# Kernel optimization log

Hardware: AMD Instinct MI355X
Metric: run time of the kernel (lower is better)

The kernel has to match this reference:

```python
import jax, jax.numpy as jnp
import numpy as np

SWIGLU_ALPHA = 1.702
SWIGLU_LIMIT = 7.0
B, S, H, E, K, I = 2, 2048, 2048, 32, 4, 1024


def setup_inputs() -> dict:
    key = jax.random.key(0)
    ks = jax.random.split(key, 8)
    return {
        "hidden_states": jax.random.normal(ks[0], (B, S, H), jnp.float32),
        "gate_w": jax.random.normal(ks[1], (E, H), jnp.float32) * 0.02,
        "gate_b": jnp.zeros((E,), jnp.float32),
        "w_gate": jax.random.normal(ks[2], (E, H, I), jnp.float32) * 0.02,
        "b_gate": jnp.zeros((E, I), jnp.float32),
        "w_up": jax.random.normal(ks[3], (E, H, I), jnp.float32) * 0.02,
        "b_up": jnp.zeros((E, I), jnp.float32),
        "w_down": jax.random.normal(ks[4], (E, I, H), jnp.float32) * 0.02,
        "b_down": jnp.zeros((E, H), jnp.float32),
    }


def reference(hidden_states, gate_w, gate_b, w_gate, b_gate, w_up, b_up, w_down, b_down):
    Bb, Ss, Hh = hidden_states.shape
    x = hidden_states.reshape(-1, Hh)                      # [T, H]
    # --- gate: top-k logits first, then softmax over the selected subset ---
    logits = x @ gate_w.T + gate_b                         # [T, E]
    topk_logits, topk_idx = jax.lax.top_k(logits, K)       # sorted descending
    topk_weight = jax.nn.softmax(topk_logits.astype(jnp.float32), axis=-1)  # [T, K]
    # --- dispatch: replicate each token K times, sort by expert id ---
    flat_idx = topk_idx.reshape(-1)                        # [T*K]
    xs = jnp.repeat(x, K, axis=0)                          # [T*K, H]
    order = jnp.argsort(flat_idx)                          # stable sort by expert
    xt = xs[order]
    gid = flat_idx[order]                                  # expert id per sorted row
    group_sizes = jnp.bincount(flat_idx, length=E).astype(jnp.int32)
    # --- grouped GEMM experts with GPT-OSS SwiGLU ---
    gate = jax.lax.ragged_dot(xt, w_gate, group_sizes) + b_gate[gid]
    up = jax.lax.ragged_dot(xt, w_up, group_sizes) + b_up[gid]
    gate = jnp.minimum(gate, SWIGLU_LIMIT)
    up = jnp.clip(up, -SWIGLU_LIMIT, SWIGLU_LIMIT)
    glu = gate * jax.nn.sigmoid(SWIGLU_ALPHA * gate)
    activated = (up + 1.0) * glu
    outs = jax.lax.ragged_dot(activated, w_down, group_sizes) + b_down[gid]
    # --- unsort and combine with routing weights ---
    inv = jnp.argsort(order)
    outs = outs[inv].reshape(-1, K, Hh)                    # [T, K, H]
    y = jnp.sum(outs * topk_weight[..., None], axis=1).astype(x.dtype)
    return y.reshape(Bb, Ss, Hh)
```

## Files before the change

### kernel.cpp

```cpp
#include <hip/hip_runtime.h>

#define T_TOK 4096
#define E_EXP 32
#define HDIM  2048
#define IDIM  1024
#define TKROW 16384
#define BM    256
#define MAXT  96

typedef __attribute__((ext_vector_type(8))) short   short8;
typedef __attribute__((ext_vector_type(8))) __bf16  bf16x8;
typedef __attribute__((ext_vector_type(4))) float   f32x4;

typedef const __attribute__((address_space(1))) unsigned int* gas_t;
typedef __attribute__((address_space(3))) unsigned int*       las_t;

static __device__ __forceinline__ void gload16(const void* g, void* l) {
    __builtin_amdgcn_global_load_lds((gas_t)(uintptr_t)g, (las_t)(uintptr_t)l, 16, 0, 0);
}

static __device__ __forceinline__ f32x4 mfma16(short8 a, short8 b, f32x4 c) {
    return __builtin_amdgcn_mfma_f32_16x16x32_bf16(
        __builtin_bit_cast(bf16x8, a), __builtin_bit_cast(bf16x8, b), c, 0, 0, 0);
}

static __device__ __forceinline__ unsigned short f2bf(float f) {
    unsigned u = __builtin_bit_cast(unsigned, f);
    unsigned r = (u + 0x7FFFu + ((u >> 16) & 1u)) >> 16;
    return (unsigned short)r;
}
static __device__ __forceinline__ float bf2f(unsigned short u) {
    return __builtin_bit_cast(float, ((unsigned)u) << 16);
}
static __device__ __forceinline__ unsigned cvtpk(float lo, float hi) {
    unsigned r;
    asm("v_cvt_pk_bf16_f32 %0, %1, %2" : "=v"(r) : "v"(lo), "v"(hi));
    return r;
}

#define VM0()   asm volatile("s_waitcnt vmcnt(0)" ::: "memory")
#define LGKM0() asm volatile("s_waitcnt lgkmcnt(0)" ::: "memory")

__global__ __launch_bounds__(256) void gating_kernel(
    const float* __restrict__ x, const float* __restrict__ gw,
    const float* __restrict__ gb, int* __restrict__ topk_idx,
    float* __restrict__ topk_w)
{
    int wave = threadIdx.x >> 6, lane = threadIdx.x & 63;
    int t = blockIdx.x * 4 + wave;
    const float* xr = x + (size_t)t * HDIM;
    float xv[32];
#pragma unroll
    for (int j = 0; j < 32; j++) xv[j] = xr[lane + 64 * j];
    float logits[E_EXP];
#pragma unroll
    for (int e = 0; e < E_EXP; e++) {
        const float* wr = gw + (size_t)e * HDIM;
        float s = 0.f;
#pragma unroll
        for (int j = 0; j < 32; j++) s = fmaf(xv[j], wr[lane + 64 * j], s);
#pragma unroll
        for (int off = 32; off; off >>= 1) s += __shfl_xor(s, off);
        logits[e] = s + gb[e];
    }
    unsigned sel = 0;
    float v[4]; int id[4];
#pragma unroll
    for (int kk = 0; kk < 4; kk++) {
        float best = -3.4e38f; int bi = 0;
#pragma unroll
        for (int e = 0; e < E_EXP; e++) {
            bool ok = ((sel >> e) & 1u) == 0u;
            bool gt = ok && (logits[e] > best);
            best = gt ? logits[e] : best;
            bi   = gt ? e : bi;
        }
        sel |= 1u << bi; v[kk] = best; id[kk] = bi;
    }
    float m0 = v[0];
    float e0 = __expf(v[0] - m0), e1 = __expf(v[1] - m0);
    float e2 = __expf(v[2] - m0), e3 = __expf(v[3] - m0);
    float inv = 1.f / (e0 + e1 + e2 + e3);
    if (lane == 0) {
        int b4 = t * 4;
        topk_idx[b4 + 0] = id[0]; topk_w[b4 + 0] = e0 * inv;
        topk_idx[b4 + 1] = id[1]; topk_w[b4 + 1] = e1 * inv;
        topk_idx[b4 + 2] = id[2]; topk_w[b4 + 2] = e2 * inv;
        topk_idx[b4 + 3] = id[3]; topk_w[b4 + 3] = e3 * inv;
    }
}

__global__ void init_kernel(int* counts, int* fill) {
    if (threadIdx.x < E_EXP) { counts[threadIdx.x] = 0; fill[threadIdx.x] = 0; }
}

__global__ void histo_kernel(const int* __restrict__ idx, int* counts) {
    int i = blockIdx.x * 256 + threadIdx.x;
    atomicAdd(&counts[idx[i]], 1);
}

__global__ void scan_tiles_kernel(const int* counts, int* offsets,
                                  int* tile_e, int* tile_r, int* ntiles) {
    if (threadIdx.x == 0) {
        int acc = 0;
        for (int e = 0; e < E_EXP; e++) { offsets[e] = acc; acc += counts[e]; }
        offsets[E_EXP] = acc;
        int nt = 0;
        for (int e = 0; e < E_EXP; e++) {
            int c = counts[e];
            for (int r = 0; r < c; r += BM) {
                tile_e[nt] = e; tile_r[nt] = offsets[e] + r; nt++;
            }
        }
        ntiles[0] = nt;
    }
}

__global__ void scatter_kernel(const int* __restrict__ idx, const int* __restrict__ offsets,
                               int* fill, int* __restrict__ pos_of, int* __restrict__ row_tok) {
    int i = blockIdx.x * 256 + threadIdx.x;
    int e = idx[i];
    int pos = offsets[e] + atomicAdd(&fill[e], 1);
    pos_of[i] = pos;
    row_tok[pos] = i >> 2;
}

__global__ __launch_bounds__(64) void gather_kernel(
    const float* __restrict__ x, const int* __restrict__ row_tok,
    unsigned short* __restrict__ xt)
{
    int r = blockIdx.x, lane = threadIdx.x;
    const f32x4* src = (const f32x4*)(x + (size_t)row_tok[r] * HDIM);
    unsigned short* dst = xt + (size_t)r * HDIM;
#pragma unroll
    for (int j = 0; j < 8; j++) {
        f32x4 f = src[lane + 64 * j];
        uint2 o;
        o.x = cvtpk(f[0], f[1]);
        o.y = cvtpk(f[2], f[3]);
        *(uint2*)(dst + 4 * (lane + 64 * j)) = o;
    }
}

__global__ __launch_bounds__(512, 2) void gemm1_kernel(
    const unsigned short* __restrict__ xt, const float* __restrict__ w_gate,
    const float* __restrict__ b_gate, const float* __restrict__ w_up,
    const float* __restrict__ b_up, const int* __restrict__ tile_e,
    const int* __restrict__ tile_r, const int* __restrict__ ntiles,
    const int* __restrict__ offsets, const int* __restrict__ counts,
    unsigned short* __restrict__ act)
{
    int flat = blockIdx.y * 8 + blockIdx.x;
    int swz = (flat & 7) * (MAXT * 8 / 8) + (flat >> 3);
    int tid = swz >> 3, nb = swz & 7;
    if (tid >= ntiles[0]) return;
    int e = tile_e[tid], row0 = tile_r[tid];
    int cnt_end = offsets[e] + counts[e];
    int n0 = nb * 128;

    __shared__ unsigned short As[2][BM * 64];
    __shared__ unsigned short Bgs[2][128 * 64];
    __shared__ unsigned short Bus[2][128 * 64];

    int t = threadIdx.x, lane = t & 63, w = t >> 6;
    int wr = w >> 2, wc = w & 3;
    int lrow = lane & 15, lg8 = (lane >> 4) * 8;

    f32x4 accg[8][2], accu[8][2];
#pragma unroll
    for (int m = 0; m < 8; m++)
#pragma unroll
        for (int n = 0; n < 2; n++) { accg[m][n] = (f32x4)0.f; accu[m][n] = (f32x4)0.f; }

    int arow_l = (lane >> 3);
    int achunk = (lane & 7) ^ arow_l;
    int bn = (t & 31) * 4, bk = (t >> 5) * 4;
    int bfswz = ((t & 31) & 7) << 3;
    size_t wB = (size_t)e * ((size_t)HDIM * IDIM) + (size_t)bk * IDIM + n0 + bn;

    f32x4 gReg[4], uReg[4];

#define G1_STAGE_A(KT, BUF) do { int k0_ = (KT) * 64; \
    _Pragma("unroll") for (int i_ = 0; i_ < 4; i_++) { \
        int ar_ = row0 + 32 * w + 8 * i_ + arow_l; \
        if (ar_ > TKROW - 1) ar_ = TKROW - 1; \
        gload16(xt + (size_t)ar_ * HDIM + k0_ + achunk * 8, \
                (void*)&As[BUF][(32 * w + 8 * i_) * 64]); \
    } } while (0)

#define G1_LOADB(KT) do { \
    const float* gp_ = w_gate + wB + (size_t)(KT) * 64 * IDIM; \
    const float* up_ = w_up   + wB + (size_t)(KT) * 64 * IDIM; \
    _Pragma("unroll") for (int kk_ = 0; kk_ < 4; kk_++) { \
        gReg[kk_] = *(const f32x4*)(gp_ + (size_t)kk_ * IDIM); \
        uReg[kk_] = *(const f32x4*)(up_ + (size_t)kk_ * IDIM); \
    } } while (0)

#define G1_WRITEB(BUF) do { \
    _Pragma("unroll") for (int j_ = 0; j_ < 4; j_++) { \
        uint2 vg_, vu_; \
        vg_.x = cvtpk(gReg[0][j_], gReg[1][j_]); vg_.y = cvtpk(gReg[2][j_], gReg[3][j_]); \
        vu_.x = cvtpk(uReg[0][j_], uReg[1][j_]); vu_.y = cvtpk(uReg[2][j_], uReg[3][j_]); \
        int d_ = (bn + j_) * 64 + (bk ^ bfswz); \
        *(uint2*)&Bgs[BUF][d_] = vg_; *(uint2*)&Bus[BUF][d_] = vu_; \
    } } while (0)

#define G1_MFMA(BUF) do { \
    __builtin_amdgcn_s_setprio(1); \
    _Pragma("unroll") for (int kk_ = 0; kk_ < 2; kk_++) { \
        short8 af_[8], bg_[2], bu_[2]; \
        int ke_ = kk_ * 32 + lg8; \
        _Pragma("unroll") for (int m_ = 0; m_ < 8; m_++) \
            af_[m_] = *(const short8*)&As[BUF][(wr * 128 + m_ * 16 + lrow) * 64 + (ke_ ^ ((lrow & 7) << 3))]; \
        _Pragma("unroll") for (int n_ = 0; n_ < 2; n_++) { \
            int rb_ = wc * 32 + n_ * 16 + lrow; \
            int d_ = rb_ * 64 + (ke_ ^ (((rb_ >> 2) & 7) << 3)); \
            bg_[n_] = *(const short8*)&Bgs[BUF][d_]; \
            bu_[n_] = *(const short8*)&Bus[BUF][d_]; \
        } \
        _Pragma("unroll") for (int m_ = 0; m_ < 8; m_++) \
        _Pragma("unroll") for (int n_ = 0; n_ < 2; n_++) { \
            accg[m_][n_] = mfma16(af_[m_], bg_[n_], accg[m_][n_]); \
            accu[m_][n_] = mfma16(af_[m_], bu_[n_], accu[m_][n_]); \
        } \
    } \
    __builtin_amdgcn_s_setprio(0); } while (0)

    G1_STAGE_A(0, 0);
    G1_LOADB(0);
    VM0();
    G1_WRITEB(0);
    LGKM0();
    __builtin_amdgcn_s_barrier();

    int cur = 0;
#pragma unroll 1
    for (int kt = 0; kt < 32; kt++) {
        if (kt + 1 < 32) { G1_STAGE_A(kt + 1, cur ^ 1); G1_LOADB(kt + 1); }
        G1_MFMA(cur);
        VM0();
        if (kt + 1 < 32) G1_WRITEB(cur ^ 1);
        LGKM0();
        __builtin_amdgcn_s_barrier();
        cur ^= 1;
    }
#undef G1_STAGE_A
#undef G1_LOADB
#undef G1_WRITEB
#undef G1_MFMA

#pragma unroll
    for (int nf = 0; nf < 2; nf++) {
        int col = n0 + wc * 32 + nf * 16 + lrow;
        float bgv = b_gate[e * IDIM + col];
        float buv = b_up[e * IDIM + col];
#pragma unroll
        for (int m = 0; m < 8; m++) {
            int rb = row0 + wr * 128 + m * 16 + (lane >> 4) * 4;
#pragma unroll
            for (int r = 0; r < 4; r++) {
                int grow = rb + r;
                if (grow < cnt_end) {
                    float gv = accg[m][nf][r] + bgv;
                    float uv = accu[m][nf][r] + buv;
                    gv = fminf(gv, 7.f);
                    uv = fminf(fmaxf(uv, -7.f), 7.f);
                    float glu = gv / (1.f + __expf(-1.702f * gv));
                    act[(size_t)grow * IDIM + col] = f2bf((uv + 1.f) * glu);
                }
            }
        }
    }
}

__global__ __launch_bounds__(512, 2) void gemm2_kernel(
    const unsigned short* __restrict__ actb, const float* __restrict__ w_down,
    const float* __restrict__ b_down, const int* __restrict__ tile_e,
    const int* __restrict__ tile_r, const int* __restrict__ ntiles,
    const int* __restrict__ offsets, const int* __restrict__ counts,
    unsigned short* __restrict__ outs)
{
    int flat = blockIdx.y * 8 + blockIdx.x;
    int swz = (flat & 7) * (MAXT * 8 / 8) + (flat >> 3);
    int tid = swz >> 3, nb = swz & 7;
    if (tid >= ntiles[0]) return;
    int e = tile_e[tid], row0 = tile_r[tid];
    int cnt_end = offsets[e] + counts[e];
    int n0 = nb * 256;

    __shared__ unsigned short As[2][BM * 64];
    __shared__ unsigned short Bs[2][256 * 64];

    int t = threadIdx.x, lane = t & 63, w = t >> 6;
    int wr = w >> 2, wc = w & 3;
    int lrow = lane & 15, lg8 = (lane >> 4) * 8;

    f32x4 acc[8][4];
#pragma unroll
    for (int m = 0; m < 8; m++)
#pragma unroll
        for (int n = 0; n < 4; n++) acc[m][n] = (f32x4)0.f;

    int arow_l = (lane >> 3);
    int achunk = (lane & 7) ^ arow_l;
    int bn = (t & 63) * 4, bk = w * 8;
    int bfswz = (lane & 7) << 3;
    size_t wB = (size_t)e * ((size_t)IDIM * HDIM) + (size_t)bk * HDIM + n0 + bn;

    f32x4 dReg[8];

#define G2_STAGE_A(KT, BUF) do { int k0_ = (KT) * 64; \
    _Pragma("unroll") for (int i_ = 0; i_ < 4; i_++) { \
        int ar_ = row0 + 32 * w + 8 * i_ + arow_l; \
        if (ar_ > TKROW - 1) ar_ = TKROW - 1; \
        gload16(actb + (size_t)ar_ * IDIM + k0_ + achunk * 8, \
                (void*)&As[BUF][(32 * w + 8 * i_) * 64]); \
    } } while (0)

#define G2_LOADB(KT) do { \
    const float* gp_ = w_down + wB + (size_t)(KT) * 64 * HDIM; \
    _Pragma("unroll") for (int kk_ = 0; kk_ < 8; kk_++) \
        dReg[kk_] = *(const f32x4*)(gp_ + (size_t)kk_ * HDIM); \
    } while (0)

#define G2_WRITEB(BUF) do { \
    _Pragma("unroll") for (int j_ = 0; j_ < 4; j_++) { \
        uint4 v_; \
        v_.x = cvtpk(dReg[0][j_], dReg[1][j_]); v_.y = cvtpk(dReg[2][j_], dReg[3][j_]); \
        v_.z = cvtpk(dReg[4][j_], dReg[5][j_]); v_.w = cvtpk(dReg[6][j_], dReg[7][j_]); \
        int d_ = (bn + j_) * 64 + (bk ^ bfswz); \
        *(uint4*)&Bs[BUF][d_] = v_; \
    } } while (0)

#define G2_MFMA(BUF) do { \
    __builtin_amdgcn_s_setprio(1); \
    _Pragma("unroll") for (int kk_ = 0; kk_ < 2; kk_++) { \
        short8 af_[8], bf_[4]; \
        int ke_ = kk_ * 32 + lg8; \
        _Pragma("unroll") for (int m_ = 0; m_ < 8; m_++) \
            af_[m_] = *(const short8*)&As[BUF][(wr * 128 + m_ * 16 + lrow) * 64 + (ke_ ^ ((lrow & 7) << 3))]; \
        _Pragma("unroll") for (int n_ = 0; n_ < 4; n_++) { \
            int rb_ = wc * 64 + n_ * 16 + lrow; \
            bf_[n_] = *(const short8*)&Bs[BUF][rb_ * 64 + (ke_ ^ (((rb_ >> 2) & 7) << 3))]; \
        } \
        _Pragma("unroll") for (int m_ = 0; m_ < 8; m_++) \
        _Pragma("unroll") for (int n_ = 0; n_ < 4; n_++) \
            acc[m_][n_] = mfma16(af_[m_], bf_[n_], acc[m_][n_]); \
    } \
    __builtin_amdgcn_s_setprio(0); } while (0)

    G2_STAGE_A(0, 0);
    G2_LOADB(0);
    VM0();
    G2_WRITEB(0);
    LGKM0();
    __builtin_amdgcn_s_barrier();

    int cur = 0;
#pragma unroll 1
    for (int kt = 0; kt < 16; kt++) {
        if (kt + 1 < 16) { G2_STAGE_A(kt + 1, cur ^ 1); G2_LOADB(kt + 1); }
        G2_MFMA(cur);
        VM0();
        if (kt + 1 < 16) G2_WRITEB(cur ^ 1);
        LGKM0();
        __builtin_amdgcn_s_barrier();
        cur ^= 1;
    }
#undef G2_STAGE_A
#undef G2_LOADB
#undef G2_WRITEB
#undef G2_MFMA

#pragma unroll
    for (int nf = 0; nf < 4; nf++) {
        int col = n0 + wc * 64 + nf * 16 + lrow;
        float bdv = b_down[e * HDIM + col];
#pragma unroll
        for (int m = 0; m < 8; m++) {
            int rb = row0 + wr * 128 + m * 16 + (lane >> 4) * 4;
#pragma unroll
            for (int r = 0; r < 4; r++) {
                int grow = rb + r;
                if (grow < cnt_end)
                    outs[(size_t)grow * HDIM + col] = f2bf(acc[m][nf][r] + bdv);
            }
        }
    }
}

__global__ __launch_bounds__(256) void combine_kernel(
    const unsigned short* __restrict__ outs, const int* __restrict__ pos_of,
    const float* __restrict__ topk_w, float* __restrict__ y)
{
    int tok = blockIdx.x;
    int c0 = threadIdx.x * 8;
    float acc[8] = {0.f, 0.f, 0.f, 0.f, 0.f, 0.f, 0.f, 0.f};
#pragma unroll
    for (int k = 0; k < 4; k++) {
        int pos = pos_of[tok * 4 + k];
        float w = topk_w[tok * 4 + k];
        short8 vv = *(const short8*)(outs + (size_t)pos * HDIM + c0);
#pragma unroll
        for (int j = 0; j < 8; j++)
            acc[j] = fmaf(w, bf2f((unsigned short)vv[j]), acc[j]);
    }
    float4 o0 = make_float4(acc[0], acc[1], acc[2], acc[3]);
    float4 o1 = make_float4(acc[4], acc[5], acc[6], acc[7]);
    *(float4*)(y + (size_t)tok * HDIM + c0)     = o0;
    *(float4*)(y + (size_t)tok * HDIM + c0 + 4) = o1;
}

extern "C" void kernel_launch(void* const* d_in, const int* in_sizes, int n_in,
                              void* d_out, int out_size, void* d_ws, size_t ws_size,
                              hipStream_t stream) {
    const float* x      = (const float*)d_in[0];
    const float* gw     = (const float*)d_in[1];
    const float* gb     = (const float*)d_in[2];
    const float* w_gate = (const float*)d_in[3];
    const float* b_gate = (const float*)d_in[4];
    const float* w_up   = (const float*)d_in[5];
    const float* b_up   = (const float*)d_in[6];
    const float* w_down = (const float*)d_in[7];
    const float* b_down = (const float*)d_in[8];
    float* y = (float*)d_out;

    char* base = (char*)d_ws;
    size_t off = 0;
    int*   topk_idx = (int*)(base + off);   off += (size_t)TKROW * 4;
    float* topk_w   = (float*)(base + off); off += (size_t)TKROW * 4;
    int*   counts   = (int*)(base + off);   off += 256;
    int*   offsets  = (int*)(base + off);   off += 256;
    int*   fill     = (int*)(base + off);   off += 256;
    int*   ntiles   = (int*)(base + off);   off += 256;
    int*   tile_e   = (int*)(base + off);   off += 1024;
    int*   tile_r   = (int*)(base + off);   off += 1024;
    int*   pos_of   = (int*)(base + off);   off += (size_t)TKROW * 4;
    int*   row_tok  = (int*)(base + off);   off += (size_t)TKROW * 4;
    unsigned short* xt   = (unsigned short*)(base + off); off += (size_t)TKROW * HDIM * 2;
    unsigned short* act  = (unsigned short*)(base + off); off += (size_t)TKROW * IDIM * 2;
    unsigned short* outs = (unsigned short*)(base + off); off += (size_t)TKROW * HDIM * 2;

    init_kernel<<<1, 64, 0, stream>>>(counts, fill);
    gating_kernel<<<T_TOK / 4, 256, 0, stream>>>(x, gw, gb, topk_idx, topk_w);
    histo_kernel<<<TKROW / 256, 256, 0, stream>>>(topk_idx, counts);
    scan_tiles_kernel<<<1, 64, 0, stream>>>(counts, offsets, tile_e, tile_r, ntiles);
    scatter_kernel<<<TKROW / 256, 256, 0, stream>>>(topk_idx, offsets, fill, pos_of, row_tok);
    gather_kernel<<<TKROW, 64, 0, stream>>>(x, row_tok, xt);
    gemm1_kernel<<<dim3(8, MAXT), 512, 0, stream>>>(
        xt, w_gate, b_gate, w_up, b_up, tile_e, tile_r, ntiles, offsets, counts, act);
    gemm2_kernel<<<dim3(8, MAXT), 512, 0, stream>>>(
        act, w_down, b_down, tile_e, tile_r, ntiles, offsets, counts, outs);
    combine_kernel<<<T_TOK, 256, 0, stream>>>(outs, pos_of, topk_w, y);
}
```

Baseline: 622.6 us.

## Halve expert GEMM N-tiles and double-buffer weight register prefetch with partial vmcnt waits

Both grouped-GEMM kernels now use half-width N tiles: 64 columns for gate/up and 128 for down. The grid is doubled and waves are rearranged into a 4x2 layout with smaller accumulator arrays. The weight fp32->bf16 staging now keeps two register sets in flight, prefetching two k-steps ahead. The full vmcnt(0) drains are replaced by counted waits, and a sched_barrier is added after each barrier, so global loads overlap MFMA work. The cost is that the A tile is re-read from memory by twice as many blocks, and the hand-counted waitcnt logic is fragile.

```diff
diff --git a/kernel.cpp b/kernel.cpp
--- a/kernel.cpp
+++ b/kernel.cpp
@@ -37,9 +37,16 @@
     asm("v_cvt_pk_bf16_f32 %0, %1, %2" : "=v"(r) : "v"(lo), "v"(hi));
     return r;
 }
-
-#define VM0()   asm volatile("s_waitcnt vmcnt(0)" ::: "memory")
-#define LGKM0() asm volatile("s_waitcnt lgkmcnt(0)" ::: "memory")
+static __device__ __forceinline__ unsigned cvtpkp(float lo, float hi) {
+    unsigned r;
+    asm volatile("v_cvt_pk_bf16_f32 %0, %1, %2" : "=v"(r) : "v"(lo), "v"(hi) : "memory");
+    return r;
+}
+
+#define FENCE()    asm volatile("" ::: "memory")
+#define WAITVM(N)  asm volatile("s_waitcnt vmcnt(" #N ")" ::: "memory")
+#define LGKM0()    asm volatile("s_waitcnt lgkmcnt(0)" ::: "memory")
+#define BAR()      do { __builtin_amdgcn_s_barrier(); __builtin_amdgcn_sched_barrier(0); } while (0)
 
 __global__ __launch_bounds__(256) void gating_kernel(
     const float* __restrict__ x, const float* __restrict__ gw,
@@ -150,35 +157,34 @@
     const int* __restrict__ offsets, const int* __restrict__ counts,
     unsigned short* __restrict__ act)
 {
-    int flat = blockIdx.y * 8 + blockIdx.x;
-    int swz = (flat & 7) * (MAXT * 8 / 8) + (flat >> 3);
-    int tid = swz >> 3, nb = swz & 7;
+    int flat = blockIdx.y * 16 + blockIdx.x;
+    int swz = (flat & 7) * 192 + (flat >> 3);
+    int tid = swz >> 4, nb = swz & 15;
     if (tid >= ntiles[0]) return;
     int e = tile_e[tid], row0 = tile_r[tid];
     int cnt_end = offsets[e] + counts[e];
-    int n0 = nb * 128;
+    int n0 = nb * 64;
 
     __shared__ unsigned short As[2][BM * 64];
-    __shared__ unsigned short Bgs[2][128 * 64];
-    __shared__ unsigned short Bus[2][128 * 64];
+    __shared__ unsigned short Bg[2][64 * 64];
+    __shared__ unsigned short Bu[2][64 * 64];
 
     int t = threadIdx.x, lane = t & 63, w = t >> 6;
-    int wr = w >> 2, wc = w & 3;
+    int wr = w >> 1, wc = w & 1;
     int lrow = lane & 15, lg8 = (lane >> 4) * 8;
 
-    f32x4 accg[8][2], accu[8][2];
-#pragma unroll
-    for (int m = 0; m < 8; m++)
+    f32x4 accg[4][2], accu[4][2];
+#pragma unroll
+    for (int m = 0; m < 4; m++)
 #pragma unroll
         for (int n = 0; n < 2; n++) { accg[m][n] = (f32x4)0.f; accu[m][n] = (f32x4)0.f; }
 
-    int arow_l = (lane >> 3);
+    int arow_l = lane >> 3;
     int achunk = (lane & 7) ^ arow_l;
-    int bn = (t & 31) * 4, bk = (t >> 5) * 4;
-    int bfswz = ((t & 31) & 7) << 3;
-    size_t wB = (size_t)e * ((size_t)HDIM * IDIM) + (size_t)bk * IDIM + n0 + bn;
-
-    f32x4 gReg[4], uReg[4];
+    int bn4 = (t & 15) * 4, kr2 = (t >> 4) * 2;
+    size_t wB = (size_t)e * ((size_t)HDIM * IDIM) + (size_t)kr2 * IDIM + n0 + bn4;
+
+    f32x4 gS0[2], uS0[2], gS1[2], uS1[2];
 
 #define G1_STAGE_A(KT, BUF) do { int k0_ = (KT) * 64; \
     _Pragma("unroll") for (int i_ = 0; i_ < 4; i_++) { \
@@ -188,62 +194,76 @@
                 (void*)&As[BUF][(32 * w + 8 * i_) * 64]); \
     } } while (0)
 
-#define G1_LOADB(KT) do { \
-    const float* gp_ = w_gate + wB + (size_t)(KT) * 64 * IDIM; \
-    const float* up_ = w_up   + wB + (size_t)(KT) * 64 * IDIM; \
-    _Pragma("unroll") for (int kk_ = 0; kk_ < 4; kk_++) { \
-        gReg[kk_] = *(const f32x4*)(gp_ + (size_t)kk_ * IDIM); \
-        uReg[kk_] = *(const f32x4*)(up_ + (size_t)kk_ * IDIM); \
-    } } while (0)
-
-#define G1_WRITEB(BUF) do { \
+#define G1_LOADB(KT, GV, UV) do { \
+    const float* gp_ = w_gate + wB + (size_t)(KT) * (64 * IDIM); \
+    const float* up_ = w_up   + wB + (size_t)(KT) * (64 * IDIM); \
+    GV[0] = *(const f32x4*)(gp_); GV[1] = *(const f32x4*)(gp_ + IDIM); \
+    UV[0] = *(const f32x4*)(up_); UV[1] = *(const f32x4*)(up_ + IDIM); \
+    } while (0)
+
+#define G1_WRITEB(GV, UV, BUF) do { \
     _Pragma("unroll") for (int j_ = 0; j_ < 4; j_++) { \
-        uint2 vg_, vu_; \
-        vg_.x = cvtpk(gReg[0][j_], gReg[1][j_]); vg_.y = cvtpk(gReg[2][j_], gReg[3][j_]); \
-        vu_.x = cvtpk(uReg[0][j_], uReg[1][j_]); vu_.y = cvtpk(uReg[2][j_], uReg[3][j_]); \
-        int d_ = (bn + j_) * 64 + (bk ^ bfswz); \
-        *(uint2*)&Bgs[BUF][d_] = vg_; *(uint2*)&Bus[BUF][d_] = vu_; \
+        unsigned vg_ = cvtpkp(GV[0][j_], GV[1][j_]); \
+        unsigned vu_ = cvtpkp(UV[0][j_], UV[1][j_]); \
+        int r_ = bn4 + j_; int d_ = r_ * 64 + (kr2 ^ ((r_ & 7) << 3)); \
+        *(unsigned*)&Bg[BUF][d_] = vg_; *(unsigned*)&Bu[BUF][d_] = vu_; \
     } } while (0)
 
 #define G1_MFMA(BUF) do { \
     __builtin_amdgcn_s_setprio(1); \
     _Pragma("unroll") for (int kk_ = 0; kk_ < 2; kk_++) { \
-        short8 af_[8], bg_[2], bu_[2]; \
+        short8 af_[4], bg_[2], bu_[2]; \
         int ke_ = kk_ * 32 + lg8; \
-        _Pragma("unroll") for (int m_ = 0; m_ < 8; m_++) \
-            af_[m_] = *(const short8*)&As[BUF][(wr * 128 + m_ * 16 + lrow) * 64 + (ke_ ^ ((lrow & 7) << 3))]; \
+        _Pragma("unroll") for (int m_ = 0; m_ < 4; m_++) { \
+            int rr_ = wr * 64 + m_ * 16 + lrow; \
+            af_[m_] = *(const short8*)&As[BUF][rr_ * 64 + (ke_ ^ ((rr_ & 7) << 3))]; } \
         _Pragma("unroll") for (int n_ = 0; n_ < 2; n_++) { \
-            int rb_ = wc * 32 + n_ * 16 + lrow; \
-            int d_ = rb_ * 64 + (ke_ ^ (((rb_ >> 2) & 7) << 3)); \
-            bg_[n_] = *(const short8*)&Bgs[BUF][d_]; \
-            bu_[n_] = *(const short8*)&Bus[BUF][d_]; \
-        } \
-        _Pragma("unroll") for (int m_ = 0; m_ < 8; m_++) \
+            int rr_ = wc * 32 + n_ * 16 + lrow; \
+            int d_ = rr_ * 64 + (ke_ ^ ((rr_ & 7) << 3)); \
+            bg_[n_] = *(const short8*)&Bg[BUF][d_]; \
+            bu_[n_] = *(const short8*)&Bu[BUF][d_]; } \
+        _Pragma("unroll") for (int m_ = 0; m_ < 4; m_++) \
         _Pragma("unroll") for (int n_ = 0; n_ < 2; n_++) { \
             accg[m_][n_] = mfma16(af_[m_], bg_[n_], accg[m_][n_]); \
-            accu[m_][n_] = mfma16(af_[m_], bu_[n_], accu[m_][n_]); \
-        } \
+            accu[m_][n_] = mfma16(af_[m_], bu_[n_], accu[m_][n_]); } \
     } \
     __builtin_amdgcn_s_setprio(0); } while (0)
 
-    G1_STAGE_A(0, 0);
-    G1_LOADB(0);
-    VM0();
-    G1_WRITEB(0);
-    LGKM0();
-    __builtin_amdgcn_s_barrier();
+    G1_STAGE_A(0, 0); FENCE();
+    G1_LOADB(0, gS0, uS0); FENCE();
+    G1_LOADB(1, gS1, uS1); FENCE();
+    WAITVM(4);
+    G1_WRITEB(gS0, uS0, 0);
+    LGKM0(); BAR();
 
     int cur = 0;
 #pragma unroll 1
-    for (int kt = 0; kt < 32; kt++) {
-        if (kt + 1 < 32) { G1_STAGE_A(kt + 1, cur ^ 1); G1_LOADB(kt + 1); }
+    for (int kt = 0; kt < 30; kt += 2) {
+        FENCE(); G1_STAGE_A(kt + 1, cur ^ 1); FENCE();
+        G1_LOADB(kt + 2, gS0, uS0); FENCE();
         G1_MFMA(cur);
-        VM0();
-        if (kt + 1 < 32) G1_WRITEB(cur ^ 1);
-        LGKM0();
-        __builtin_amdgcn_s_barrier();
+        WAITVM(8);
+        G1_WRITEB(gS1, uS1, cur ^ 1);
+        WAITVM(4);
+        LGKM0(); BAR();
         cur ^= 1;
-    }
+        FENCE(); G1_STAGE_A(kt + 2, cur ^ 1); FENCE();
+        G1_LOADB(kt + 3, gS1, uS1); FENCE();
+        G1_MFMA(cur);
+        WAITVM(8);
+        G1_WRITEB(gS0, uS0, cur ^ 1);
+        WAITVM(4);
+        LGKM0(); BAR();
+        cur ^= 1;
+    }
+    FENCE(); G1_STAGE_A(31, cur ^ 1); FENCE();
+    G1_MFMA(cur);
+    WAITVM(4);
+    G1_WRITEB(gS1, uS1, cur ^ 1);
+    WAITVM(0);
+    LGKM0(); BAR();
+    cur ^= 1;
+    G1_MFMA(cur);
 #undef G1_STAGE_A
 #undef G1_LOADB
 #undef G1_WRITEB
@@ -255,8 +275,8 @@
         float bgv = b_gate[e * IDIM + col];
         float buv = b_up[e * IDIM + col];
 #pragma unroll
-        for (int m = 0; m < 8; m++) {
-            int rb = row0 + wr * 128 + m * 16 + (lane >> 4) * 4;
+        for (int m = 0; m < 4; m++) {
+            int rb = row0 + wr * 64 + m * 16 + (lane >> 4) * 4;
 #pragma unroll
             for (int r = 0; r < 4; r++) {
                 int grow = rb + r;
@@ -280,34 +300,33 @@
     const int* __restrict__ offsets, const int* __restrict__ counts,
     unsigned short* __restrict__ outs)
 {
-    int flat = blockIdx.y * 8 + blockIdx.x;
-    int swz = (flat & 7) * (MAXT * 8 / 8) + (flat >> 3);
-    int tid = swz >> 3, nb = swz & 7;
+    int flat = blockIdx.y * 16 + blockIdx.x;
+    int swz = (flat & 7) * 192 + (flat >> 3);
+    int tid = swz >> 4, nb = swz & 15;
     if (tid >= ntiles[0]) return;
     int e = tile_e[tid], row0 = tile_r[tid];
     int cnt_end = offsets[e] + counts[e];
-    int n0 = nb * 256;
+    int n0 = nb * 128;
 
     __shared__ unsigned short As[2][BM * 64];
-    __shared__ unsigned short Bs[2][256 * 64];
+    __shared__ unsigned short Bs[2][128 * 64];
 
     int t = threadIdx.x, lane = t & 63, w = t >> 6;
-    int wr = w >> 2, wc = w & 3;
+    int wr = w >> 1, wc = w & 1;
     int lrow = lane & 15, lg8 = (lane >> 4) * 8;
 
-    f32x4 acc[8][4];
-#pragma unroll
-    for (int m = 0; m < 8; m++)
+    f32x4 acc[4][4];
+#pragma unroll
+    for (int m = 0; m < 4; m++)
 #pragma unroll
         for (int n = 0; n < 4; n++) acc[m][n] = (f32x4)0.f;
 
-    int arow_l = (lane >> 3);
+    int arow_l = lane >> 3;
     int achunk = (lane & 7) ^ arow_l;
-    int bn = (t & 63) * 4, bk = w * 8;
-    int bfswz = (lane & 7) << 3;
-    size_t wB = (size_t)e * ((size_t)IDIM * HDIM) + (size_t)bk * HDIM + n0 + bn;
-
-    f32x4 dReg[8];
+    int bn4 = (t & 31) * 4, kr4 = (t >> 5) * 4;
+    size_t wB = (size_t)e * ((size_t)IDIM * HDIM) + (size_t)kr4 * HDIM + n0 + bn4;
+
+    f32x4 dS0[4], dS1[4];
 
 #define G2_STAGE_A(KT, BUF) do { int k0_ = (KT) * 64; \
     _Pragma("unroll") for (int i_ = 0; i_ < 4; i_++) { \
@@ -317,56 +336,72 @@
                 (void*)&As[BUF][(32 * w + 8 * i_) * 64]); \
     } } while (0)
 
-#define G2_LOADB(KT) do { \
-    const float* gp_ = w_down + wB + (size_t)(KT) * 64 * HDIM; \
-    _Pragma("unroll") for (int kk_ = 0; kk_ < 8; kk_++) \
-        dReg[kk_] = *(const f32x4*)(gp_ + (size_t)kk_ * HDIM); \
+#define G2_LOADB(KT, DV) do { \
+    const float* gp_ = w_down + wB + (size_t)(KT) * (64 * HDIM); \
+    DV[0] = *(const f32x4*)(gp_);            DV[1] = *(const f32x4*)(gp_ + HDIM); \
+    DV[2] = *(const f32x4*)(gp_ + 2 * HDIM); DV[3] = *(const f32x4*)(gp_ + 3 * HDIM); \
     } while (0)
 
-#define G2_WRITEB(BUF) do { \
+#define G2_WRITEB(DV, BUF) do { \
     _Pragma("unroll") for (int j_ = 0; j_ < 4; j_++) { \
-        uint4 v_; \
-        v_.x = cvtpk(dReg[0][j_], dReg[1][j_]); v_.y = cvtpk(dReg[2][j_], dReg[3][j_]); \
-        v_.z = cvtpk(dReg[4][j_], dReg[5][j_]); v_.w = cvtpk(dReg[6][j_], dReg[7][j_]); \
-        int d_ = (bn + j_) * 64 + (bk ^ bfswz); \
-        *(uint4*)&Bs[BUF][d_] = v_; \
+        uint2 v_; \
+        v_.x = cvtpkp(DV[0][j_], DV[1][j_]); v_.y = cvtpkp(DV[2][j_], DV[3][j_]); \
+        int r_ = bn4 + j_; int d_ = r_ * 64 + (kr4 ^ ((r_ & 7) << 3)); \
+        *(uint2*)&Bs[BUF][d_] = v_; \
     } } while (0)
 
 #define G2_MFMA(BUF) do { \
     __builtin_amdgcn_s_setprio(1); \
     _Pragma("unroll") for (int kk_ = 0; kk_ < 2; kk_++) { \
-        short8 af_[8], bf_[4]; \
+        short8 af_[4], bf_[4]; \
         int ke_ = kk_ * 32 + lg8; \
-        _Pragma("unroll") for (int m_ = 0; m_ < 8; m_++) \
-            af_[m_] = *(const short8*)&As[BUF][(wr * 128 + m_ * 16 + lrow) * 64 + (ke_ ^ ((lrow & 7) << 3))]; \
+        _Pragma("unroll") for (int m_ = 0; m_ < 4; m_++) { \
+            int rr_ = wr * 64 + m_ * 16 + lrow; \
+            af_[m_] = *(const short8*)&As[BUF][rr_ * 64 + (ke_ ^ ((rr_ & 7) << 3))]; } \
         _Pragma("unroll") for (int n_ = 0; n_ < 4; n_++) { \
-            int rb_ = wc * 64 + n_ * 16 + lrow; \
-            bf_[n_] = *(const short8*)&Bs[BUF][rb_ * 64 + (ke_ ^ (((rb_ >> 2) & 7) << 3))]; \
-        } \
-        _Pragma("unroll") for (int m_ = 0; m_ < 8; m_++) \
+            int rr_ = wc * 64 + n_ * 16 + lrow; \
+            bf_[n_] = *(const short8*)&Bs[BUF][rr_ * 64 + (ke_ ^ ((rr_ & 7) << 3))]; } \
+        _Pragma("unroll") for (int m_ = 0; m_ < 4; m_++) \
         _Pragma("unroll") for (int n_ = 0; n_ < 4; n_++) \
             acc[m_][n_] = mfma16(af_[m_], bf_[n_], acc[m_][n_]); \
     } \
     __builtin_amdgcn_s_setprio(0); } while (0)
 
-    G2_STAGE_A(0, 0);
-    G2_LOADB(0);
-    VM0();
-    G2_WRITEB(0);
-    LGKM0();
-    __builtin_amdgcn_s_barrier();
+    G2_STAGE_A(0, 0); FENCE();
+    G2_LOADB(0, dS0); FENCE();
+    G2_LOADB(1, dS1); FENCE();
+    WAITVM(4);
+    G2_WRITEB(dS0, 0);
+    LGKM0(); BAR();
 
     int cur = 0;
 #pragma unroll 1
-    for (int kt = 0; kt < 16; kt++) {
-        if (kt + 1 < 16) { G2_STAGE_A(kt + 1, cur ^ 1); G2_LOADB(kt + 1); }
+    for (int kt = 0; kt < 14; kt += 2) {
+        FENCE(); G2_STAGE_A(kt + 1, cur ^ 1); FENCE();
+        G2_LOADB(kt + 2, dS0); FENCE();
         G2_MFMA(cur);
-        VM0();
-        if (kt + 1 < 16) G2_WRITEB(cur ^ 1);
-        LGKM0();
-        __builtin_amdgcn_s_barrier();
+        WAITVM(8);
+        G2_WRITEB(dS1, cur ^ 1);
+        WAITVM(4);
+        LGKM0(); BAR();
         cur ^= 1;
-    }
+        FENCE(); G2_STAGE_A(kt + 2, cur ^ 1); FENCE();
+        G2_LOADB(kt + 3, dS1); FENCE();
+        G2_MFMA(cur);
+        WAITVM(8);
+        G2_WRITEB(dS0, cur ^ 1);
+        WAITVM(4);
+        LGKM0(); BAR();
+        cur ^= 1;
+    }
+    FENCE(); G2_STAGE_A(15, cur ^ 1); FENCE();
+    G2_MFMA(cur);
+    WAITVM(4);
+    G2_WRITEB(dS1, cur ^ 1);
+    WAITVM(0);
+    LGKM0(); BAR();
+    cur ^= 1;
+    G2_MFMA(cur);
 #undef G2_STAGE_A
 #undef G2_LOADB
 #undef G2_WRITEB
@@ -377,8 +412,8 @@
         int col = n0 + wc * 64 + nf * 16 + lrow;
         float bdv = b_down[e * HDIM + col];
 #pragma unroll
-        for (int m = 0; m < 8; m++) {
-            int rb = row0 + wr * 128 + m * 16 + (lane >> 4) * 4;
+        for (int m = 0; m < 4; m++) {
+            int rb = row0 + wr * 64 + m * 16 + (lane >> 4) * 4;
 #pragma unroll
             for (int r = 0; r < 4; r++) {
                 int grow = rb + r;
@@ -447,9 +482,9 @@
     scan_tiles_kernel<<<1, 64, 0, stream>>>(counts, offsets, tile_e, tile_r, ntiles);
     scatter_kernel<<<TKROW / 256, 256, 0, stream>>>(topk_idx, offsets, fill, pos_of, row_tok);
     gather_kernel<<<TKROW, 64, 0, stream>>>(x, row_tok, xt);
-    gemm1_kernel<<<dim3(8, MAXT), 512, 0, stream>>>(
+    gemm1_kernel<<<dim3(16, MAXT), 512, 0, stream>>>(
         xt, w_gate, b_gate, w_up, b_up, tile_e, tile_r, ntiles, offsets, counts, act);
-    gemm2_kernel<<<dim3(8, MAXT), 512, 0, stream>>>(
+    gemm2_kernel<<<dim3(16, MAXT), 512, 0, stream>>>(
         act, w_down, b_down, tile_e, tile_r, ntiles, offsets, counts, outs);
     combine_kernel<<<T_TOK, 256, 0, stream>>>(outs, pos_of, topk_w, y);
 }
```

After: 716.8 us. 15.1% more time.

## Deepen B-weight register prefetch to two stages and split MFMA halves around LDS writes

Applied to the files above, without the earlier changes.

Both grouped GEMM kernels now keep two register sets of fp32 weights in flight, loading tile kt+2 while tile kt is computed. Each k-tile's MFMA work is split into two halves, with the bf16 conversion and LDS write of the next B tile placed between them. Partial vmcnt waits replace full drains, and compiler fences plus sched_barrier pin the ordering. This aims to hide global weight-load latency behind MFMA work, at the cost of more VGPRs (possible spills or lower occupancy under launch_bounds(512,2)) and fragile hand-counted waitcnt values.

```diff
diff --git a/kernel.cpp b/kernel.cpp
--- a/kernel.cpp
+++ b/kernel.cpp
@@ -37,9 +37,16 @@
     asm("v_cvt_pk_bf16_f32 %0, %1, %2" : "=v"(r) : "v"(lo), "v"(hi));
     return r;
 }
-
-#define VM0()   asm volatile("s_waitcnt vmcnt(0)" ::: "memory")
-#define LGKM0() asm volatile("s_waitcnt lgkmcnt(0)" ::: "memory")
+static __device__ __forceinline__ unsigned cvtpkp(float lo, float hi) {
+    unsigned r;
+    asm volatile("v_cvt_pk_bf16_f32 %0, %1, %2" : "=v"(r) : "v"(lo), "v"(hi) : "memory");
+    return r;
+}
+
+#define FENCE()    asm volatile("" ::: "memory")
+#define WAITVM(N)  asm volatile("s_waitcnt vmcnt(" #N ")" ::: "memory")
+#define LGKM0()    asm volatile("s_waitcnt lgkmcnt(0)" ::: "memory")
+#define BAR()      do { __builtin_amdgcn_s_barrier(); __builtin_amdgcn_sched_barrier(0); } while (0)
 
 __global__ __launch_bounds__(256) void gating_kernel(
     const float* __restrict__ x, const float* __restrict__ gw,
@@ -151,7 +158,7 @@
     unsigned short* __restrict__ act)
 {
     int flat = blockIdx.y * 8 + blockIdx.x;
-    int swz = (flat & 7) * (MAXT * 8 / 8) + (flat >> 3);
+    int swz = (flat & 7) * (MAXT) + (flat >> 3);
     int tid = swz >> 3, nb = swz & 7;
     if (tid >= ntiles[0]) return;
     int e = tile_e[tid], row0 = tile_r[tid];
@@ -178,7 +185,7 @@
     int bfswz = ((t & 31) & 7) << 3;
     size_t wB = (size_t)e * ((size_t)HDIM * IDIM) + (size_t)bk * IDIM + n0 + bn;
 
-    f32x4 gReg[4], uReg[4];
+    f32x4 gS0[4], uS0[4], gS1[4], uS1[4];
 
 #define G1_STAGE_A(KT, BUF) do { int k0_ = (KT) * 64; \
     _Pragma("unroll") for (int i_ = 0; i_ < 4; i_++) { \
@@ -188,28 +195,28 @@
                 (void*)&As[BUF][(32 * w + 8 * i_) * 64]); \
     } } while (0)
 
-#define G1_LOADB(KT) do { \
+#define G1_LOADB(KT, GV, UV) do { \
     const float* gp_ = w_gate + wB + (size_t)(KT) * 64 * IDIM; \
     const float* up_ = w_up   + wB + (size_t)(KT) * 64 * IDIM; \
     _Pragma("unroll") for (int kk_ = 0; kk_ < 4; kk_++) { \
-        gReg[kk_] = *(const f32x4*)(gp_ + (size_t)kk_ * IDIM); \
-        uReg[kk_] = *(const f32x4*)(up_ + (size_t)kk_ * IDIM); \
+        GV[kk_] = *(const f32x4*)(gp_ + (size_t)kk_ * IDIM); \
+        UV[kk_] = *(const f32x4*)(up_ + (size_t)kk_ * IDIM); \
     } } while (0)
 
-#define G1_WRITEB(BUF) do { \
+#define G1_WRITEB(GV, UV, BUF) do { \
     _Pragma("unroll") for (int j_ = 0; j_ < 4; j_++) { \
         uint2 vg_, vu_; \
-        vg_.x = cvtpk(gReg[0][j_], gReg[1][j_]); vg_.y = cvtpk(gReg[2][j_], gReg[3][j_]); \
-        vu_.x = cvtpk(uReg[0][j_], uReg[1][j_]); vu_.y = cvtpk(uReg[2][j_], uReg[3][j_]); \
+        vg_.x = cvtpkp(GV[0][j_], GV[1][j_]); vg_.y = cvtpkp(GV[2][j_], GV[3][j_]); \
+        vu_.x = cvtpkp(UV[0][j_], UV[1][j_]); vu_.y = cvtpkp(UV[2][j_], UV[3][j_]); \
         int d_ = (bn + j_) * 64 + (bk ^ bfswz); \
         *(uint2*)&Bgs[BUF][d_] = vg_; *(uint2*)&Bus[BUF][d_] = vu_; \
     } } while (0)
 
-#define G1_MFMA(BUF) do { \
+#define G1_MFMA_H(BUF, KK) do { \
     __builtin_amdgcn_s_setprio(1); \
-    _Pragma("unroll") for (int kk_ = 0; kk_ < 2; kk_++) { \
+    { \
         short8 af_[8], bg_[2], bu_[2]; \
-        int ke_ = kk_ * 32 + lg8; \
+        int ke_ = (KK) * 32 + lg8; \
         _Pragma("unroll") for (int m_ = 0; m_ < 8; m_++) \
             af_[m_] = *(const short8*)&As[BUF][(wr * 128 + m_ * 16 + lrow) * 64 + (ke_ ^ ((lrow & 7) << 3))]; \
         _Pragma("unroll") for (int n_ = 0; n_ < 2; n_++) { \
@@ -226,28 +233,46 @@
     } \
     __builtin_amdgcn_s_setprio(0); } while (0)
 
-    G1_STAGE_A(0, 0);
-    G1_LOADB(0);
-    VM0();
-    G1_WRITEB(0);
-    LGKM0();
-    __builtin_amdgcn_s_barrier();
+    G1_STAGE_A(0, 0); FENCE();
+    G1_LOADB(0, gS0, uS0); FENCE();
+    G1_LOADB(1, gS1, uS1); FENCE();
+    WAITVM(8);
+    G1_WRITEB(gS0, uS0, 0);
+    LGKM0(); BAR();
 
     int cur = 0;
 #pragma unroll 1
-    for (int kt = 0; kt < 32; kt++) {
-        if (kt + 1 < 32) { G1_STAGE_A(kt + 1, cur ^ 1); G1_LOADB(kt + 1); }
-        G1_MFMA(cur);
-        VM0();
-        if (kt + 1 < 32) G1_WRITEB(cur ^ 1);
-        LGKM0();
-        __builtin_amdgcn_s_barrier();
-        cur ^= 1;
-    }
+    for (int kt = 0; kt < 30; kt += 2) {
+        FENCE(); G1_STAGE_A(kt + 1, cur ^ 1); FENCE();
+        G1_LOADB(kt + 2, gS0, uS0); FENCE();
+        G1_MFMA_H(cur, 0);
+        WAITVM(12);
+        G1_WRITEB(gS1, uS1, cur ^ 1);
+        G1_MFMA_H(cur, 1);
+        WAITVM(8);
+        LGKM0(); BAR(); cur ^= 1;
+        FENCE(); G1_STAGE_A(kt + 2, cur ^ 1); FENCE();
+        G1_LOADB(kt + 3, gS1, uS1); FENCE();
+        G1_MFMA_H(cur, 0);
+        WAITVM(12);
+        G1_WRITEB(gS0, uS0, cur ^ 1);
+        G1_MFMA_H(cur, 1);
+        WAITVM(8);
+        LGKM0(); BAR(); cur ^= 1;
+    }
+    FENCE(); G1_STAGE_A(31, cur ^ 1); FENCE();
+    G1_MFMA_H(cur, 0);
+    WAITVM(4);
+    G1_WRITEB(gS1, uS1, cur ^ 1);
+    G1_MFMA_H(cur, 1);
+    WAITVM(0);
+    LGKM0(); BAR(); cur ^= 1;
+    G1_MFMA_H(cur, 0);
+    G1_MFMA_H(cur, 1);
 #undef G1_STAGE_A
 #undef G1_LOADB
 #undef G1_WRITEB
-#undef G1_MFMA
+#undef G1_MFMA_H
 
 #pragma unroll
     for (int nf = 0; nf < 2; nf++) {
@@ -281,7 +306,7 @@
     unsigned short* __restrict__ outs)
 {
     int flat = blockIdx.y * 8 + blockIdx.x;
-    int swz = (flat & 7) * (MAXT * 8 / 8) + (flat >> 3);
+    int swz = (flat & 7) * (MAXT) + (flat >> 3);
     int tid = swz >> 3, nb = swz & 7;
     if (tid >= ntiles[0]) return;
     int e = tile_e[tid], row0 = tile_r[tid];
@@ -307,7 +332,7 @@
     int bfswz = (lane & 7) << 3;
     size_t wB = (size_t)e * ((size_t)IDIM * HDIM) + (size_t)bk * HDIM + n0 + bn;
 
-    f32x4 dReg[8];
+    f32x4 dS0[8], dS1[8];
 
 #define G2_STAGE_A(KT, BUF) do { int k0_ = (KT) * 64; \
     _Pragma("unroll") for (int i_ = 0; i_ < 4; i_++) { \
@@ -317,26 +342,26 @@
                 (void*)&As[BUF][(32 * w + 8 * i_) * 64]); \
     } } while (0)
 
-#define G2_LOADB(KT) do { \
+#define G2_LOADB(KT, DV) do { \
     const float* gp_ = w_down + wB + (size_t)(KT) * 64 * HDIM; \
     _Pragma("unroll") for (int kk_ = 0; kk_ < 8; kk_++) \
-        dReg[kk_] = *(const f32x4*)(gp_ + (size_t)kk_ * HDIM); \
+        DV[kk_] = *(const f32x4*)(gp_ + (size_t)kk_ * HDIM); \
     } while (0)
 
-#define G2_WRITEB(BUF) do { \
+#define G2_WRITEB(DV, BUF) do { \
     _Pragma("unroll") for (int j_ = 0; j_ < 4; j_++) { \
         uint4 v_; \
-        v_.x = cvtpk(dReg[0][j_], dReg[1][j_]); v_.y = cvtpk(dReg[2][j_], dReg[3][j_]); \
-        v_.z = cvtpk(dReg[4][j_], dReg[5][j_]); v_.w = cvtpk(dReg[6][j_], dReg[7][j_]); \
+        v_.x = cvtpkp(DV[0][j_], DV[1][j_]); v_.y = cvtpkp(DV[2][j_], DV[3][j_]); \
+        v_.z = cvtpkp(DV[4][j_], DV[5][j_]); v_.w = cvtpkp(DV[6][j_], DV[7][j_]); \
         int d_ = (bn + j_) * 64 + (bk ^ bfswz); \
         *(uint4*)&Bs[BUF][d_] = v_; \
     } } while (0)
 
-#define G2_MFMA(BUF) do { \
+#define G2_MFMA_H(BUF, KK) do { \
     __builtin_amdgcn_s_setprio(1); \
-    _Pragma("unroll") for (int kk_ = 0; kk_ < 2; kk_++) { \
+    { \
         short8 af_[8], bf_[4]; \
-        int ke_ = kk_ * 32 + lg8; \
+        int ke_ = (KK) * 32 + lg8; \
         _Pragma("unroll") for (int m_ = 0; m_ < 8; m_++) \
             af_[m_] = *(const short8*)&As[BUF][(wr * 128 + m_ * 16 + lrow) * 64 + (ke_ ^ ((lrow & 7) << 3))]; \
         _Pragma("unroll") for (int n_ = 0; n_ < 4; n_++) { \
@@ -349,28 +374,46 @@
     } \
     __builtin_amdgcn_s_setprio(0); } while (0)
 
-    G2_STAGE_A(0, 0);
-    G2_LOADB(0);
-    VM0();
-    G2_WRITEB(0);
-    LGKM0();
-    __builtin_amdgcn_s_barrier();
+    G2_STAGE_A(0, 0); FENCE();
+    G2_LOADB(0, dS0); FENCE();
+    G2_LOADB(1, dS1); FENCE();
+    WAITVM(8);
+    G2_WRITEB(dS0, 0);
+    LGKM0(); BAR();
 
     int cur = 0;
 #pragma unroll 1
-    for (int kt = 0; kt < 16; kt++) {
-        if (kt + 1 < 16) { G2_STAGE_A(kt + 1, cur ^ 1); G2_LOADB(kt + 1); }
-        G2_MFMA(cur);
-        VM0();
-        if (kt + 1 < 16) G2_WRITEB(cur ^ 1);
-        LGKM0();
-        __builtin_amdgcn_s_barrier();
-        cur ^= 1;
-    }
+    for (int kt = 0; kt < 14; kt += 2) {
+        FENCE(); G2_STAGE_A(kt + 1, cur ^ 1); FENCE();
+        G2_LOADB(kt + 2, dS0); FENCE();
+        G2_MFMA_H(cur, 0);
+        WAITVM(12);
+        G2_WRITEB(dS1, cur ^ 1);
+        G2_MFMA_H(cur, 1);
+        WAITVM(8);
+        LGKM0(); BAR(); cur ^= 1;
+        FENCE(); G2_STAGE_A(kt + 2, cur ^ 1); FENCE();
+        G2_LOADB(kt + 3, dS1); FENCE();
+        G2_MFMA_H(cur, 0);
+        WAITVM(12);
+        G2_WRITEB(dS0, cur ^ 1);
+        G2_MFMA_H(cur, 1);
+        WAITVM(8);
+        LGKM0(); BAR(); cur ^= 1;
+    }
+    FENCE(); G2_STAGE_A(15, cur ^ 1); FENCE();
+    G2_MFMA_H(cur, 0);
+    WAITVM(4);
+    G2_WRITEB(dS1, cur ^ 1);
+    G2_MFMA_H(cur, 1);
+    WAITVM(0);
+    LGKM0(); BAR(); cur ^= 1;
+    G2_MFMA_H(cur, 0);
+    G2_MFMA_H(cur, 1);
 #undef G2_STAGE_A
 #undef G2_LOADB
 #undef G2_WRITEB
-#undef G2_MFMA
+#undef G2_MFMA_H
 
 #pragma unroll
     for (int nf = 0; nf < 4; nf++) {
```

Result: slower. 636.5 us (+2.2%).
